# Performance work log

Measured on AMD Instinct MI355X. Metric: run time of the kernel, lower is better.

The kernel has to match this reference:

```python
import jax, jax.numpy as jnp
import numpy as np

EMB = 1024
HEADS = 16
HEAD_SIZE = EMB // HEADS  # 64
B, T = 2, 2048


def setup_inputs() -> dict:
    key = jax.random.key(0)
    k1, k2, k3 = jax.random.split(key, 3)
    x = jax.random.normal(k1, (B, T, EMB), dtype=jnp.float32)
    # scale weights like typical init to keep logits sane
    w_qkv = jax.random.normal(k2, (EMB, 3 * EMB), dtype=jnp.float32) * (EMB ** -0.5)
    w_proj = jax.random.normal(k3, (EMB, EMB), dtype=jnp.float32) * (EMB ** -0.5)
    b_proj = jnp.zeros((EMB,), dtype=jnp.float32)
    return {"x": x, "w_qkv": w_qkv, "w_proj": w_proj, "b_proj": b_proj}


def reference(x, w_qkv, w_proj, b_proj):
    Bb, Tt, C = x.shape
    qkv = x @ w_qkv  # [B,T,3C]
    q, k, v = jnp.split(qkv, 3, axis=-1)
    # [B,H,T,hs]
    q = q.reshape(Bb, Tt, HEADS, HEAD_SIZE).transpose(0, 2, 1, 3)
    k = k.reshape(Bb, Tt, HEADS, HEAD_SIZE).transpose(0, 2, 1, 3)
    v = v.reshape(Bb, Tt, HEADS, HEAD_SIZE).transpose(0, 2, 1, 3)
    scale = HEAD_SIZE ** -0.5
    wei = jnp.einsum('bhqd,bhkd->bhqk', q, k) * scale  # [B,H,T,T]
    causal = jnp.tril(jnp.ones((Tt, Tt), dtype=bool))
    wei = jnp.where(causal, wei, -jnp.inf)
    wei = jax.nn.softmax(wei, axis=-1)
    out = jnp.einsum('bhqk,bhkd->bhqd', wei, v)  # [B,H,T,hs]
    out = out.transpose(0, 2, 1, 3).reshape(Bb, Tt, C)
    out = out @ w_proj + b_proj
    return out
```

## Files before the change

kernel.cpp:

```cpp
#include <hip/hip_runtime.h>
#include <hip/hip_bf16.h>

typedef __attribute__((ext_vector_type(8))) short short8;
typedef __attribute__((ext_vector_type(4))) float floatx4;

#define MFMA16(a, b, c) __builtin_amdgcn_mfma_f32_16x16x32_bf16((a), (b), (c), 0, 0, 0)
#define GLOBAL_AS __attribute__((address_space(1)))
#define LDS_AS __attribute__((address_space(3)))

__device__ __forceinline__ unsigned short f2bf(float x) {
  union { float f; unsigned u; } v; v.f = x;
  unsigned r = v.u + 0x7FFFu + ((v.u >> 16) & 1u);
  return (unsigned short)(r >> 16);
}

__device__ __forceinline__ short8 ld8(const unsigned short* p) {
  return *reinterpret_cast<const short8*>(p);
}

__device__ __forceinline__ void async_cp16(const unsigned short* g, unsigned short* l) {
  __builtin_amdgcn_global_load_lds((const GLOBAL_AS void*)g, (LDS_AS void*)l, 16, 0, 0);
}

__global__ __launch_bounds__(256) void k_prep(
    const float* __restrict__ x, unsigned short* __restrict__ xb,
    const float* __restrict__ w_qkv, unsigned short* __restrict__ wqkvT,
    const float* __restrict__ w_proj, unsigned short* __restrict__ wprojT) {
  __shared__ float tile[64][65];
  int bid = blockIdx.x, tid = threadIdx.x;
  if (bid < 4096) {
    int i = bid * 256 + tid;
    float4 f = reinterpret_cast<const float4*>(x)[i];
    union { unsigned short u[4]; unsigned long long v; } o;
    o.u[0] = f2bf(f.x); o.u[1] = f2bf(f.y); o.u[2] = f2bf(f.z); o.u[3] = f2bf(f.w);
    reinterpret_cast<unsigned long long*>(xb)[i] = o.v;
    return;
  }
  const float* in; unsigned short* out; int R, C, bx, by;
  if (bid < 4864) {
    int rel = bid - 4096;
    in = w_qkv; out = wqkvT; R = 1024; C = 3072; bx = rel % 48; by = rel / 48;
  } else {
    int rel = bid - 4864;
    in = w_proj; out = wprojT; R = 1024; C = 1024; bx = rel % 16; by = rel / 16;
  }
  int tx = tid & 63, ty = tid >> 6;
  int c0 = bx * 64, r0 = by * 64;
  for (int i = ty; i < 64; i += 4)
    tile[i][tx] = in[(size_t)(r0 + i) * C + c0 + tx];
  __syncthreads();
  for (int i = ty; i < 64; i += 4)
    out[(size_t)(c0 + i) * R + r0 + tx] = f2bf(tile[tx][i]);
}

__global__ __launch_bounds__(256) void k_gemm_qkv(
    const unsigned short* __restrict__ A, const unsigned short* __restrict__ Bt,
    unsigned short* __restrict__ qk, unsigned short* __restrict__ vT, int K) {
  __shared__ unsigned short As[128][64];
  __shared__ unsigned short Bs[128][64];
  int tid = threadIdx.x;
  int w = tid >> 6, lane = tid & 63, quad = lane >> 4, l16 = lane & 15;
  int wy = w >> 1, wx = w & 1;
  int rowB = blockIdx.y * 128, colB = blockIdx.x * 128;
  int srcRow = lane >> 3;
  int srcCol = (((lane & 7) ^ (srcRow & 7)) << 3);

  floatx4 acc[4][4];
  floatx4 zero4 = {0.f, 0.f, 0.f, 0.f};
#pragma unroll
  for (int mi = 0; mi < 4; ++mi)
#pragma unroll
    for (int ni = 0; ni < 4; ++ni) acc[mi][ni] = zero4;

  for (int kt = 0; kt < K; kt += 64) {
    __syncthreads();
#pragma unroll
    for (int i = 0; i < 4; ++i) {
      int r0 = w * 32 + i * 8;
      async_cp16(&A[(size_t)(rowB + r0 + srcRow) * K + kt + srcCol], &As[r0][0]);
      async_cp16(&Bt[(size_t)(colB + r0 + srcRow) * K + kt + srcCol], &Bs[r0][0]);
    }
    __syncthreads();
#pragma unroll
    for (int kh = 0; kh < 2; ++kh) {
      short8 af[4], bf_[4];
#pragma unroll
      for (int mi = 0; mi < 4; ++mi)
        af[mi] = ld8(&As[wy * 64 + mi * 16 + l16][((kh * 4 + quad) ^ (l16 & 7)) << 3]);
#pragma unroll
      for (int ni = 0; ni < 4; ++ni)
        bf_[ni] = ld8(&Bs[wx * 64 + ni * 16 + l16][((kh * 4 + quad) ^ (l16 & 7)) << 3]);
#pragma unroll
      for (int mi = 0; mi < 4; ++mi)
#pragma unroll
        for (int ni = 0; ni < 4; ++ni)
          acc[mi][ni] = MFMA16(af[mi], bf_[ni], acc[mi][ni]);
    }
  }

  if (colB < 2048) {
#pragma unroll
    for (int mi = 0; mi < 4; ++mi) {
      int row = rowB + wy * 64 + mi * 16 + quad * 4;
#pragma unroll
      for (int ni = 0; ni < 4; ++ni) {
        int col = colB + wx * 64 + ni * 16 + l16;
#pragma unroll
        for (int r = 0; r < 4; ++r)
          qk[(size_t)(row + r) * 2048 + col] = f2bf(acc[mi][ni][r]);
      }
    }
  } else {
#pragma unroll
    for (int mi = 0; mi < 4; ++mi) {
      int row = rowB + wy * 64 + mi * 16 + quad * 4;
      int b = row >> 11, t = row & 2047;
#pragma unroll
      for (int ni = 0; ni < 4; ++ni) {
        int hd = colB - 2048 + wx * 64 + ni * 16 + l16;
        union { unsigned short u[4]; unsigned long long v; } o;
#pragma unroll
        for (int r = 0; r < 4; ++r) o.u[r] = f2bf(acc[mi][ni][r]);
        *reinterpret_cast<unsigned long long*>(
            &vT[((size_t)(b * 16) * 64 + hd) * 2048 + t]) = o.v;
      }
    }
  }
}

__global__ __launch_bounds__(256) void k_gemm_proj(
    const unsigned short* __restrict__ A, const unsigned short* __restrict__ Bt,
    float* __restrict__ Cout, const float* __restrict__ bias, int M, int N, int K) {
  __shared__ unsigned short As[128][64];
  __shared__ unsigned short Bs[64][64];
  int tid = threadIdx.x;
  int w = tid >> 6, lane = tid & 63, quad = lane >> 4, l16 = lane & 15;
  int rowB = blockIdx.y * 128, colB = blockIdx.x * 64;
  int srcRow = lane >> 3;
  int srcCol = (((lane & 7) ^ (srcRow & 7)) << 3);

  floatx4 acc[2][4];
  floatx4 zero4 = {0.f, 0.f, 0.f, 0.f};
#pragma unroll
  for (int mi = 0; mi < 2; ++mi)
#pragma unroll
    for (int ni = 0; ni < 4; ++ni) acc[mi][ni] = zero4;

  for (int kt = 0; kt < K; kt += 64) {
    __syncthreads();
#pragma unroll
    for (int i = 0; i < 4; ++i) {
      int r0 = w * 32 + i * 8;
      async_cp16(&A[(size_t)(rowB + r0 + srcRow) * K + kt + srcCol], &As[r0][0]);
    }
#pragma unroll
    for (int i = 0; i < 2; ++i) {
      int r0 = w * 16 + i * 8;
      async_cp16(&Bt[(size_t)(colB + r0 + srcRow) * K + kt + srcCol], &Bs[r0][0]);
    }
    __syncthreads();
#pragma unroll
    for (int kh = 0; kh < 2; ++kh) {
      short8 af[2], bf_[4];
#pragma unroll
      for (int mi = 0; mi < 2; ++mi)
        af[mi] = ld8(&As[w * 32 + mi * 16 + l16][((kh * 4 + quad) ^ (l16 & 7)) << 3]);
#pragma unroll
      for (int ni = 0; ni < 4; ++ni)
        bf_[ni] = ld8(&Bs[ni * 16 + l16][((kh * 4 + quad) ^ (l16 & 7)) << 3]);
#pragma unroll
      for (int mi = 0; mi < 2; ++mi)
#pragma unroll
        for (int ni = 0; ni < 4; ++ni)
          acc[mi][ni] = MFMA16(af[mi], bf_[ni], acc[mi][ni]);
    }
  }

#pragma unroll
  for (int mi = 0; mi < 2; ++mi) {
    int row = rowB + w * 32 + mi * 16 + quad * 4;
#pragma unroll
    for (int ni = 0; ni < 4; ++ni) {
      int col = colB + ni * 16 + l16;
      float bv = bias[col];
#pragma unroll
      for (int r = 0; r < 4; ++r)
        Cout[(size_t)(row + r) * N + col] = acc[mi][ni][r] + bv;
    }
  }
}

__global__ __launch_bounds__(256) void k_attn(
    const unsigned short* __restrict__ qk, const unsigned short* __restrict__ vT,
    unsigned short* __restrict__ attn_out) {
  const int T = 2048, LD = 2048;
  __shared__ unsigned short Kt[64][72];
  __shared__ unsigned short Vt[64][72];
  __shared__ unsigned short Pt[4][16][76];

  int idx = blockIdx.x;
  int s = idx >> 3;
  int r = s >> 5, p = s & 31;
  int pp = (r & 2) ? ((p + 16) & 31) : p;
  int j = (r & 1) ? (31 - pp) : pp;
  int bh = (idx & 7) * 4 + r;
  int b = bh >> 4, h = bh & 15;
  int tid = threadIdx.x, w = tid >> 6, lane = tid & 63;
  int quad = lane >> 4, l16 = lane & 15;

  const unsigned short* Qp = qk + (size_t)b * T * LD + h * 64;
  const unsigned short* Kp = Qp + 1024;
  const unsigned short* Vp = vT + (size_t)bh * 64 * T;

  int q0 = j * 64;
  int nt = j + 1;

  short8 aq[2];
  {
    const unsigned short* qrow = Qp + (size_t)(q0 + w * 16 + l16) * LD + quad * 8;
    aq[0] = ld8(qrow);
    aq[1] = ld8(qrow + 32);
  }

  short8 ones8;
  {
    unsigned short o = 0x3F80;
#pragma unroll
    for (int i = 0; i < 8; ++i) ones8[i] = (short)o;
  }

  const float cscale = 0.125f * 1.44269504f;
  floatx4 o_acc[4], l_acc;
  floatx4 zero4 = {0.f, 0.f, 0.f, 0.f};
  l_acc = zero4;
#pragma unroll
  for (int nd = 0; nd < 4; ++nd) o_acc[nd] = zero4;

  int skR = tid >> 3, skC = (tid & 7) << 3;

  short8 kreg[2], vreg[2];
#pragma unroll
  for (int i = 0; i < 2; ++i) {
    kreg[i] = ld8(&Kp[(size_t)(skR + i * 32) * LD + skC]);
    vreg[i] = ld8(&Vp[(size_t)(skR + i * 32) * T + skC]);
  }

  for (int half = 0; half < nt; ++half) {
    __syncthreads();
#pragma unroll
    for (int i = 0; i < 2; ++i) {
      *reinterpret_cast<short8*>(&Kt[skR + i * 32][skC]) = kreg[i];
      *reinterpret_cast<short8*>(&Vt[skR + i * 32][skC]) = vreg[i];
    }
    __syncthreads();

    if (half + 1 < nt) {
      int key0n = (half + 1) * 64;
#pragma unroll
      for (int i = 0; i < 2; ++i) {
        kreg[i] = ld8(&Kp[(size_t)(key0n + skR + i * 32) * LD + skC]);
        vreg[i] = ld8(&Vp[(size_t)(skR + i * 32) * T + key0n + skC]);
      }
    }

    int key0 = half * 64;

    floatx4 st[4];
#pragma unroll
    for (int kt4 = 0; kt4 < 4; ++kt4) {
      short8 ak0 = ld8(&Kt[kt4 * 16 + l16][quad * 8]);
      short8 ak1 = ld8(&Kt[kt4 * 16 + l16][32 + quad * 8]);
      st[kt4] = MFMA16(ak0, aq[0], zero4);
      st[kt4] = MFMA16(ak1, aq[1], st[kt4]);
    }

    if (half == j) {
      int qlane = q0 + w * 16 + l16;
#pragma unroll
      for (int kt4 = 0; kt4 < 4; ++kt4)
#pragma unroll
        for (int rr = 0; rr < 4; ++rr)
          if (key0 + kt4 * 16 + quad * 4 + rr > qlane) st[kt4][rr] = -1e30f;
    }

#pragma unroll
    for (int kt4 = 0; kt4 < 4; ++kt4) {
      unsigned u[4];
#pragma unroll
      for (int rr = 0; rr < 4; ++rr) {
        float pe = __builtin_amdgcn_exp2f(fmaf(st[kt4][rr], cscale, -16.f));
        u[rr] = __float_as_uint(pe) + 0x8000u;
      }
      unsigned lo = __builtin_amdgcn_perm(u[1], u[0], 0x07060302u);
      unsigned hi = __builtin_amdgcn_perm(u[3], u[2], 0x07060302u);
      unsigned long long pv = ((unsigned long long)hi << 32) | lo;
      *reinterpret_cast<unsigned long long*>(
          &Pt[w][l16][kt4 * 16 + quad * 4]) = pv;
    }

    short8 pa0 = ld8(&Pt[w][l16][quad * 8]);
    short8 pa1 = ld8(&Pt[w][l16][32 + quad * 8]);
#pragma unroll
    for (int nd = 0; nd < 4; ++nd) {
      short8 bv0 = ld8(&Vt[nd * 16 + l16][quad * 8]);
      short8 bv1 = ld8(&Vt[nd * 16 + l16][32 + quad * 8]);
      o_acc[nd] = MFMA16(pa0, bv0, o_acc[nd]);
      o_acc[nd] = MFMA16(pa1, bv1, o_acc[nd]);
    }
    l_acc = MFMA16(pa0, ones8, l_acc);
    l_acc = MFMA16(pa1, ones8, l_acc);
  }

#pragma unroll
  for (int nd = 0; nd < 4; ++nd)
#pragma unroll
    for (int rr = 0; rr < 4; ++rr) {
      int q = q0 + w * 16 + quad * 4 + rr;
      int d = nd * 16 + l16;
      attn_out[(size_t)(b * T + q) * 1024 + h * 64 + d] =
          f2bf(o_acc[nd][rr] / l_acc[rr]);
    }
}

extern "C" void kernel_launch(void* const* d_in, const int* in_sizes, int n_in,
                              void* d_out, int out_size, void* d_ws, size_t ws_size,
                              hipStream_t stream) {
  const float* x = (const float*)d_in[0];
  const float* w_qkv = (const float*)d_in[1];
  const float* w_proj = (const float*)d_in[2];
  const float* b_proj = (const float*)d_in[3];
  float* out = (float*)d_out;

  char* ws = (char*)d_ws;
  unsigned short* xb     = (unsigned short*)(ws);
  unsigned short* wqkvT  = (unsigned short*)(ws + (size_t)(8  << 20));
  unsigned short* wprojT = (unsigned short*)(ws + (size_t)(14 << 20));
  unsigned short* qkb    = (unsigned short*)(ws + (size_t)(16 << 20));
  unsigned short* attnb  = (unsigned short*)(ws + (size_t)(32 << 20));
  unsigned short* vTb    = (unsigned short*)(ws + (size_t)(40 << 20));

  k_prep<<<5120, 256, 0, stream>>>(x, xb, w_qkv, wqkvT, w_proj, wprojT);
  k_gemm_qkv<<<dim3(3072 / 128, 4096 / 128), 256, 0, stream>>>(
      xb, wqkvT, qkb, vTb, 1024);
  k_attn<<<1024, 256, 0, stream>>>(qkb, vTb, attnb);
  k_gemm_proj<<<dim3(1024 / 64, 4096 / 128), 256, 0, stream>>>(
      attnb, wprojT, out, b_proj, 4096, 1024, 1024);
}
```

Measured before the change: 183.7 us.

## Split long causal attention query tiles across two blocks with atomic-counter merge

Query tiles 16-31 of the causal attention are split into two key-range halves processed by separate blocks, raising the grid from 1024 to 1536 blocks. A constant ordering table schedules the longest work first. Each half writes unnormalized fp32 partial outputs and row sums to workspace, and the last-arriving block, found with an atomic counter reset in k_prep, sums both halves and normalizes. This targets load imbalance from the triangular causal work at the cost of extra global traffic, a fence and an atomic per split tile.

```diff
diff --git a/kernel.cpp b/kernel.cpp
--- a/kernel.cpp
+++ b/kernel.cpp
@@ -22,12 +22,22 @@
   __builtin_amdgcn_global_load_lds((const GLOBAL_AS void*)g, (LDS_AS void*)l, 16, 0, 0);
 }
 
+__constant__ int ORD48[48] = {
+    15, 44, 46, 47,  14, 40, 42, 43, 45,  13, 36, 38, 39, 41,
+    12, 32, 34, 35, 37,  11, 28, 30, 31, 33,  10, 24, 26, 27, 29,
+    9, 20, 22, 23, 25,  8, 16, 18, 19, 21,  7, 17,  6, 5, 4, 3, 2, 1, 0};
+
 __global__ __launch_bounds__(256) void k_prep(
     const float* __restrict__ x, unsigned short* __restrict__ xb,
     const float* __restrict__ w_qkv, unsigned short* __restrict__ wqkvT,
-    const float* __restrict__ w_proj, unsigned short* __restrict__ wprojT) {
+    const float* __restrict__ w_proj, unsigned short* __restrict__ wprojT,
+    int* __restrict__ counters) {
   __shared__ float tile[64][65];
   int bid = blockIdx.x, tid = threadIdx.x;
+  if (bid == 0) {
+    counters[tid] = 0;
+    counters[tid + 256] = 0;
+  }
   if (bid < 4096) {
     int i = bid * 256 + tid;
     float4 f = reinterpret_cast<const float4*>(x)[i];
@@ -192,28 +202,38 @@
 
 __global__ __launch_bounds__(256) void k_attn(
     const unsigned short* __restrict__ qk, const unsigned short* __restrict__ vT,
-    unsigned short* __restrict__ attn_out) {
+    unsigned short* __restrict__ attn_out,
+    float* __restrict__ o_part, float* __restrict__ l_part,
+    int* __restrict__ counters) {
   const int T = 2048, LD = 2048;
   __shared__ unsigned short Kt[64][72];
   __shared__ unsigned short Vt[64][72];
   __shared__ unsigned short Pt[4][16][76];
+  __shared__ int done;
 
   int idx = blockIdx.x;
-  int s = idx >> 3;
-  int r = s >> 5, p = s & 31;
-  int pp = (r & 2) ? ((p + 16) & 31) : p;
-  int j = (r & 1) ? (31 - pp) : pp;
+  int g = idx >> 3;
+  int r = g & 3, o = g >> 2;
+  int c = ORD48[o];
   int bh = (idx & 7) * 4 + r;
   int b = bh >> 4, h = bh & 15;
   int tid = threadIdx.x, w = tid >> 6, lane = tid & 63;
   int quad = lane >> 4, l16 = lane & 15;
 
+  int j, h0, h1, hf = 0, pid = 0;
+  if (c < 16) {
+    j = c; h0 = 0; h1 = j + 1;
+  } else {
+    int s = c - 16; j = 16 + (s >> 1); hf = s & 1;
+    int nt = j + 1, hs = (nt + 1) >> 1;
+    h0 = hf ? hs : 0; h1 = hf ? nt : hs;
+    pid = bh * 16 + (j - 16);
+  }
+  int q0 = j * 64;
+
   const unsigned short* Qp = qk + (size_t)b * T * LD + h * 64;
   const unsigned short* Kp = Qp + 1024;
   const unsigned short* Vp = vT + (size_t)bh * 64 * T;
-
-  int q0 = j * 64;
-  int nt = j + 1;
 
   short8 aq[2];
   {
@@ -224,9 +244,9 @@
 
   short8 ones8;
   {
-    unsigned short o = 0x3F80;
-#pragma unroll
-    for (int i = 0; i < 8; ++i) ones8[i] = (short)o;
+    unsigned short oo = 0x3F80;
+#pragma unroll
+    for (int i = 0; i < 8; ++i) ones8[i] = (short)oo;
   }
 
   const float cscale = 0.125f * 1.44269504f;
@@ -241,11 +261,11 @@
   short8 kreg[2], vreg[2];
 #pragma unroll
   for (int i = 0; i < 2; ++i) {
-    kreg[i] = ld8(&Kp[(size_t)(skR + i * 32) * LD + skC]);
-    vreg[i] = ld8(&Vp[(size_t)(skR + i * 32) * T + skC]);
-  }
-
-  for (int half = 0; half < nt; ++half) {
+    kreg[i] = ld8(&Kp[(size_t)(h0 * 64 + skR + i * 32) * LD + skC]);
+    vreg[i] = ld8(&Vp[(size_t)(skR + i * 32) * T + h0 * 64 + skC]);
+  }
+
+  for (int half = h0; half < h1; ++half) {
     __syncthreads();
 #pragma unroll
     for (int i = 0; i < 2; ++i) {
@@ -254,7 +274,7 @@
     }
     __syncthreads();
 
-    if (half + 1 < nt) {
+    if (half + 1 < h1) {
       int key0n = (half + 1) * 64;
 #pragma unroll
       for (int i = 0; i < 2; ++i) {
@@ -311,15 +331,59 @@
     l_acc = MFMA16(pa1, ones8, l_acc);
   }
 
+  if (c < 16) {
+#pragma unroll
+    for (int nd = 0; nd < 4; ++nd)
+#pragma unroll
+      for (int rr = 0; rr < 4; ++rr) {
+        int q = q0 + w * 16 + quad * 4 + rr;
+        int d = nd * 16 + l16;
+        attn_out[(size_t)(b * T + q) * 1024 + h * 64 + d] =
+            f2bf(o_acc[nd][rr] / l_acc[rr]);
+      }
+    return;
+  }
+
+  int slot = pid * 2 + hf;
+  float* OP = o_part + (size_t)slot * 4096;
+  float* LP = l_part + (size_t)slot * 64;
 #pragma unroll
   for (int nd = 0; nd < 4; ++nd)
 #pragma unroll
-    for (int rr = 0; rr < 4; ++rr) {
-      int q = q0 + w * 16 + quad * 4 + rr;
-      int d = nd * 16 + l16;
-      attn_out[(size_t)(b * T + q) * 1024 + h * 64 + d] =
-          f2bf(o_acc[nd][rr] / l_acc[rr]);
-    }
+    for (int rr = 0; rr < 4; ++rr)
+      OP[(w * 16 + quad * 4 + rr) * 64 + nd * 16 + l16] = o_acc[nd][rr];
+  if (l16 == 0)
+#pragma unroll
+    for (int rr = 0; rr < 4; ++rr)
+      LP[w * 16 + quad * 4 + rr] = l_acc[rr];
+
+  __threadfence();
+  __syncthreads();
+  if (tid == 0) done = atomicAdd(&counters[pid], 1);
+  __syncthreads();
+  if (done != 1) return;
+
+  __threadfence();
+  const float* PA = o_part + (size_t)(pid * 2) * 4096;
+  const float* PB = PA + 4096;
+  const float* LA = l_part + (size_t)(pid * 2) * 64;
+  const float* LB = LA + 64;
+#pragma unroll
+  for (int pass = 0; pass < 4; ++pass) {
+    int q = pass * 16 + (tid >> 4);
+    int d0 = (tid & 15) * 4;
+    int off = q * 64 + d0;
+    float4 a = *reinterpret_cast<const float4*>(&PA[off]);
+    float4 cc = *reinterpret_cast<const float4*>(&PB[off]);
+    float rl = 1.0f / (LA[q] + LB[q]);
+    union { unsigned short u[4]; unsigned long long v; } ob;
+    ob.u[0] = f2bf((a.x + cc.x) * rl);
+    ob.u[1] = f2bf((a.y + cc.y) * rl);
+    ob.u[2] = f2bf((a.z + cc.z) * rl);
+    ob.u[3] = f2bf((a.w + cc.w) * rl);
+    *reinterpret_cast<unsigned long long*>(
+        &attn_out[(size_t)(b * T + q0 + q) * 1024 + h * 64 + d0]) = ob.v;
+  }
 }
 
 extern "C" void kernel_launch(void* const* d_in, const int* in_sizes, int n_in,
@@ -338,11 +402,14 @@
   unsigned short* qkb    = (unsigned short*)(ws + (size_t)(16 << 20));
   unsigned short* attnb  = (unsigned short*)(ws + (size_t)(32 << 20));
   unsigned short* vTb    = (unsigned short*)(ws + (size_t)(40 << 20));
-
-  k_prep<<<5120, 256, 0, stream>>>(x, xb, w_qkv, wqkvT, w_proj, wprojT);
+  float*          o_part = (float*)(ws + (size_t)(48 << 20));
+  float*          l_part = (float*)(ws + (size_t)(64 << 20));
+  int*            counters = (int*)(ws + (size_t)(64 << 20) + (512 << 10));
+
+  k_prep<<<5120, 256, 0, stream>>>(x, xb, w_qkv, wqkvT, w_proj, wprojT, counters);
   k_gemm_qkv<<<dim3(3072 / 128, 4096 / 128), 256, 0, stream>>>(
       xb, wqkvT, qkb, vTb, 1024);
-  k_attn<<<1024, 256, 0, stream>>>(qkb, vTb, attnb);
+  k_attn<<<1536, 256, 0, stream>>>(qkb, vTb, attnb, o_part, l_part, counters);
   k_gemm_proj<<<dim3(1024 / 64, 4096 / 128), 256, 0, stream>>>(
       attnb, wprojT, out, b_proj, 4096, 1024, 1024);
 }
```

New measurement: 362.7 us. +97.5%, slower.
